# Performance work log

Measured on AMD Instinct MI355X. Metric: run time of the kernel, lower is better.

## Reference

```python
import jax, jax.numpy as jnp
import numpy as np

N_ENS = 4        # number of FGL sub-layers
B, N_IN, N_OUT = 1, 16384, 4096
IN_C, OUT_C = 16, 16
DENSITY = 0.10   # sparsity proxy for A + dA random perturbation


def setup_inputs() -> dict:
    key = jax.random.key(0)
    kx, ka, km, kw, kb = jax.random.split(key, 5)
    x = jax.random.normal(kx, (B, N_IN, IN_C), dtype=jnp.float32)
    # Dense storage of the n perturbed sparse adjacencies A_i (n_out, n_in)
    A_vals = jax.random.normal(ka, (N_ENS, N_OUT, N_IN), dtype=jnp.float32)
    A_mask = jax.random.bernoulli(km, DENSITY, (N_ENS, N_OUT, N_IN))
    As = A_vals * A_mask.astype(jnp.float32)
    Ws = jax.random.normal(kw, (N_ENS, IN_C, OUT_C), dtype=jnp.float32) * (1.0 / np.sqrt(IN_C))
    bs = jax.random.normal(kb, (N_ENS, OUT_C), dtype=jnp.float32) * 0.01
    return {"x": x, "As": As, "Ws": Ws, "bs": bs}


def reference(x, As, Ws, bs):
    # Each FGL_i: y_i = (A_i @ x) @ W_i + b_i
    # x: [b, n_in, f]; As: [n, n_out, n_in]; Ws: [n, f, g]; bs: [n, g]
    h = jnp.einsum('noi,bif->nbof', As, x)            # graph aggregation per ensemble member
    y = jnp.einsum('nbof,nfg->nbog', h, Ws)           # per-member linear transform
    y = y + bs[:, None, None, :]
    return jnp.mean(y, axis=0)                        # sum over n members / n
```

## Files before the change

### kernel.cpp

```cpp
#include <hip/hip_runtime.h>


#define N_ENS 4
#define N_OUT 4096
#define N_IN  16384
#define ROWS  (N_ENS * N_OUT)
#define GSPLIT 32
#define ICHUNK (N_IN / GSPLIT)

__global__ __launch_bounds__(256, 6) void k_main(const float* __restrict__ A,
                                                 const float* __restrict__ x,
                                                 float* __restrict__ hp) {
    const int split  = blockIdx.x & (GSPLIT - 1);
    const int rowblk = blockIdx.x >> 5;
    const int row = rowblk * 256 + threadIdx.x;
    const int i0 = split * ICHUNK;

    const float* Ap  = A + (size_t)row * N_IN + i0;
    const float* xp0 = x + (size_t)i0 * 16;

    float acc[16];
#pragma unroll
    for (int f = 0; f < 16; ++f) acc[f] = 0.0f;

    for (int s = 0; s < ICHUNK / 16; ++s) {
        float4 av4[4];
#pragma unroll
        for (int q = 0; q < 4; ++q)
            av4[q] = *(const float4*)(Ap + s * 16 + q * 4);
        const float* af = (const float*)av4;
        const float* xp = xp0 + (size_t)s * 256;

#pragma unroll
        for (int ii = 0; ii < 16; ++ii) {
            const float av = af[ii];
#pragma unroll
            for (int f = 0; f < 16; ++f)
                acc[f] = fmaf(av, xp[ii * 16 + f], acc[f]);
        }
    }

    float* outp = hp + ((size_t)split * ROWS + row) * 16;
#pragma unroll
    for (int f = 0; f < 16; ++f) outp[f] = acc[f];
}

__global__ __launch_bounds__(256) void k_hsum(const float* __restrict__ hp,
                                              float* __restrict__ h) {
    int t = blockIdx.x * 256 + threadIdx.x;
    float s = 0.0f;
#pragma unroll
    for (int sp = 0; sp < GSPLIT; ++sp)
        s += hp[(size_t)sp * (ROWS * 16) + t];
    h[t] = s;
}

__global__ __launch_bounds__(256) void k_out(const float* __restrict__ h,
                                             const float* __restrict__ Ws,
                                             const float* __restrict__ bs,
                                             float* __restrict__ out) {
    __shared__ float Wsm[N_ENS * 16 * 16];
    __shared__ float bsm[N_ENS * 16];
    int tid = threadIdx.x;
#pragma unroll
    for (int r = 0; r < 4; ++r) Wsm[tid + 256 * r] = Ws[tid + 256 * r];
    if (tid < 64) bsm[tid] = bs[tid];
    __syncthreads();

    int idx = blockIdx.x * 256 + tid;
    int o = idx >> 4;
    int gg = idx & 15;
    float s = 0.0f;
#pragma unroll
    for (int n = 0; n < N_ENS; ++n) {
        const float* hr = h + ((size_t)(n * N_OUT + o) << 4);
        float t = 0.0f;
#pragma unroll
        for (int f = 0; f < 16; ++f)
            t = fmaf(hr[f], Wsm[n * 256 + f * 16 + gg], t);
        s += t + bsm[n * 16 + gg];
    }
    out[idx] = 0.25f * s;
}

extern "C" void kernel_launch(void* const* d_in, const int* in_sizes, int n_in,
                              void* d_out, int out_size, void* d_ws, size_t ws_size,
                              hipStream_t stream) {
    const float* x  = (const float*)d_in[0];
    const float* As = (const float*)d_in[1];
    const float* Ws = (const float*)d_in[2];
    const float* bs = (const float*)d_in[3];
    float* out = (float*)d_out;

    float* hp = (float*)d_ws;
    float* h  = (float*)((char*)d_ws + (size_t)32 * 1024 * 1024);

    k_main<<<64 * GSPLIT, 256, 0, stream>>>(As, x, hp);
    k_hsum<<<(ROWS * 16) / 256, 256, 0, stream>>>(hp, h);
    k_out<<<(N_OUT * 16) / 256, 256, 0, stream>>>(h, Ws, bs, out);
}
```

Baseline: 1.415 ms.

## Split each row across four lanes and reduce split count for partial sums

Remaps k_main so four lanes cooperate on one adjacency row, each loading a float4 slice, then combines the partial accumulators with wave shuffles. It reduces the i-dimension split from 32 to 8, which shrinks the partial-sum buffer written by k_main and read by k_hsum. x is read as float4 vectors. The cost is extra shuffle work and a per-lane branch to select the output slice.

```diff
diff --git a/kernel.cpp b/kernel.cpp
--- a/kernel.cpp
+++ b/kernel.cpp
@@ -5,44 +5,59 @@
 #define N_OUT 4096
 #define N_IN  16384
 #define ROWS  (N_ENS * N_OUT)
-#define GSPLIT 32
+#define GSPLIT 8
 #define ICHUNK (N_IN / GSPLIT)
+#define NSTEP  (ICHUNK / 16)
 
-__global__ __launch_bounds__(256, 6) void k_main(const float* __restrict__ A,
+__global__ __launch_bounds__(256, 4) void k_main(const float* __restrict__ A,
                                                  const float* __restrict__ x,
                                                  float* __restrict__ hp) {
-    const int split  = blockIdx.x & (GSPLIT - 1);
-    const int rowblk = blockIdx.x >> 5;
-    const int row = rowblk * 256 + threadIdx.x;
-    const int i0 = split * ICHUNK;
+    const int split   = blockIdx.x & (GSPLIT - 1);
+    const int rowtile = blockIdx.x >> 3;
+    const int tid  = threadIdx.x;
+    const int wave = tid >> 6;
+    const int r    = (tid >> 2) & 15;
+    const int p    = tid & 3;
 
-    const float* Ap  = A + (size_t)row * N_IN + i0;
-    const float* xp0 = x + (size_t)i0 * 16;
+    const int row = rowtile * 64 + wave * 16 + r;
+    const int i0  = split * ICHUNK;
+
+    const float* Ap = A + (size_t)row * N_IN + i0 + (p << 2);
 
     float acc[16];
 #pragma unroll
     for (int f = 0; f < 16; ++f) acc[f] = 0.0f;
 
-    for (int s = 0; s < ICHUNK / 16; ++s) {
-        float4 av4[4];
+    for (int s = 0; s < NSTEP; ++s) {
+        float4 av = *(const float4*)(Ap + s * 16);
+        const float* xb = x + ((size_t)(i0 + s * 16 + (p << 2)) << 4);
+        const float* af = (const float*)&av;
 #pragma unroll
-        for (int q = 0; q < 4; ++q)
-            av4[q] = *(const float4*)(Ap + s * 16 + q * 4);
-        const float* af = (const float*)av4;
-        const float* xp = xp0 + (size_t)s * 256;
-
+        for (int q = 0; q < 4; ++q) {
+            const float a = af[q];
 #pragma unroll
-        for (int ii = 0; ii < 16; ++ii) {
-            const float av = af[ii];
-#pragma unroll
-            for (int f = 0; f < 16; ++f)
-                acc[f] = fmaf(av, xp[ii * 16 + f], acc[f]);
+            for (int j = 0; j < 4; ++j) {
+                float4 xv = *(const float4*)(xb + (q << 4) + (j << 2));
+                acc[4 * j + 0] = fmaf(a, xv.x, acc[4 * j + 0]);
+                acc[4 * j + 1] = fmaf(a, xv.y, acc[4 * j + 1]);
+                acc[4 * j + 2] = fmaf(a, xv.z, acc[4 * j + 2]);
+                acc[4 * j + 3] = fmaf(a, xv.w, acc[4 * j + 3]);
+            }
         }
     }
 
-    float* outp = hp + ((size_t)split * ROWS + row) * 16;
 #pragma unroll
-    for (int f = 0; f < 16; ++f) outp[f] = acc[f];
+    for (int f = 0; f < 16; ++f) {
+        acc[f] += __shfl_xor(acc[f], 1, 64);
+        acc[f] += __shfl_xor(acc[f], 2, 64);
+    }
+
+    float4 v;
+    if      (p == 0) v = make_float4(acc[0],  acc[1],  acc[2],  acc[3]);
+    else if (p == 1) v = make_float4(acc[4],  acc[5],  acc[6],  acc[7]);
+    else if (p == 2) v = make_float4(acc[8],  acc[9],  acc[10], acc[11]);
+    else             v = make_float4(acc[12], acc[13], acc[14], acc[15]);
+    *(float4*)(hp + (((size_t)split * ROWS + row) << 4) + (p << 2)) = v;
 }
 
 __global__ __launch_bounds__(256) void k_hsum(const float* __restrict__ hp,
@@ -93,9 +108,9 @@
     float* out = (float*)d_out;
 
     float* hp = (float*)d_ws;
-    float* h  = (float*)((char*)d_ws + (size_t)32 * 1024 * 1024);
+    float* h  = (float*)((char*)d_ws + (size_t)8 * 1024 * 1024);
 
-    k_main<<<64 * GSPLIT, 256, 0, stream>>>(As, x, hp);
+    k_main<<<256 * GSPLIT, 256, 0, stream>>>(As, x, hp);
     k_hsum<<<(ROWS * 16) / 256, 256, 0, stream>>>(hp, h);
     k_out<<<(N_OUT * 16) / 256, 256, 0, stream>>>(h, Ws, bs, out);
 }
```

Measured after the change: 2.894 ms. 104% more time.

## Stage x chunk in LDS and remap threads to 4 rows by 4 features

Applied to the files above, without the earlier changes.

The main GEMV-like kernel now copies its 512x16 slice of x into shared memory once per block. Each lane computes 4 rows by 4 output features instead of one row by 16, reading A with float4 loads and prefetching the next step into registers. This is meant to cut redundant global reads of x and spread the accumulators across lanes. The trade is a 32KB LDS footprint and a lower occupancy hint (4 instead of 6). Each wave's A reads are now strided across 16 rows, which may hurt coalescing.

```diff
diff --git a/kernel.cpp b/kernel.cpp
--- a/kernel.cpp
+++ b/kernel.cpp
@@ -7,42 +7,79 @@
 #define ROWS  (N_ENS * N_OUT)
 #define GSPLIT 32
 #define ICHUNK (N_IN / GSPLIT)
+#define NSTEP  (ICHUNK / 4)
 
-__global__ __launch_bounds__(256, 6) void k_main(const float* __restrict__ A,
+__global__ __launch_bounds__(256, 4) void k_main(const float* __restrict__ A,
                                                  const float* __restrict__ x,
                                                  float* __restrict__ hp) {
-    const int split  = blockIdx.x & (GSPLIT - 1);
-    const int rowblk = blockIdx.x >> 5;
-    const int row = rowblk * 256 + threadIdx.x;
-    const int i0 = split * ICHUNK;
+    __shared__ float xs[ICHUNK * 16];
 
-    const float* Ap  = A + (size_t)row * N_IN + i0;
-    const float* xp0 = x + (size_t)i0 * 16;
+    const int split   = blockIdx.x & (GSPLIT - 1);
+    const int rowblk  = blockIdx.x >> 5;
+    const int tid  = threadIdx.x;
+    const int i0   = split * ICHUNK;
 
-    float acc[16];
+    {
+        const float4* xg = (const float4*)(x + (size_t)i0 * 16);
+        float4* xs4 = (float4*)xs;
 #pragma unroll
-    for (int f = 0; f < 16; ++f) acc[f] = 0.0f;
+        for (int j = 0; j < 8; ++j)
+            xs4[tid + 256 * j] = xg[tid + 256 * j];
+    }
+    __syncthreads();
 
-    for (int s = 0; s < ICHUNK / 16; ++s) {
-        float4 av4[4];
+    const int wave  = tid >> 6;
+    const int lane  = tid & 63;
+    const int o_sub = lane & 15;
+    const int f_sub = lane >> 4;
+    const int rowbase = rowblk * 256 + wave * 64 + o_sub;
+
+    const float* Ap = A + (size_t)rowbase * N_IN + i0;
+
+    float4 acc[4];
+#pragma unroll
+    for (int k = 0; k < 4; ++k) acc[k] = make_float4(0.f, 0.f, 0.f, 0.f);
+
+    float4 a_cur[4], a_nxt[4];
+#pragma unroll
+    for (int k = 0; k < 4; ++k)
+        a_cur[k] = *(const float4*)(Ap + (size_t)k * 16 * N_IN);
+
+#pragma unroll 2
+    for (int s = 0; s < NSTEP; ++s) {
+        if (s + 1 < NSTEP) {
+#pragma unroll
+            for (int k = 0; k < 4; ++k)
+                a_nxt[k] = *(const float4*)(Ap + (size_t)k * 16 * N_IN + (s + 1) * 4);
+        }
+
+        float4 xv[4];
 #pragma unroll
         for (int q = 0; q < 4; ++q)
-            av4[q] = *(const float4*)(Ap + s * 16 + q * 4);
-        const float* af = (const float*)av4;
-        const float* xp = xp0 + (size_t)s * 256;
+            xv[q] = *(const float4*)&xs[(s * 4 + q) * 16 + f_sub * 4];
 
 #pragma unroll
-        for (int ii = 0; ii < 16; ++ii) {
-            const float av = af[ii];
+        for (int k = 0; k < 4; ++k) {
+            const float* af = (const float*)&a_cur[k];
 #pragma unroll
-            for (int f = 0; f < 16; ++f)
-                acc[f] = fmaf(av, xp[ii * 16 + f], acc[f]);
+            for (int q = 0; q < 4; ++q) {
+                const float a = af[q];
+                acc[k].x = fmaf(a, xv[q].x, acc[k].x);
+                acc[k].y = fmaf(a, xv[q].y, acc[k].y);
+                acc[k].z = fmaf(a, xv[q].z, acc[k].z);
+                acc[k].w = fmaf(a, xv[q].w, acc[k].w);
+            }
         }
+
+#pragma unroll
+        for (int k = 0; k < 4; ++k) a_cur[k] = a_nxt[k];
     }
 
-    float* outp = hp + ((size_t)split * ROWS + row) * 16;
 #pragma unroll
-    for (int f = 0; f < 16; ++f) outp[f] = acc[f];
+    for (int k = 0; k < 4; ++k) {
+        int row = rowbase + 16 * k;
+        *(float4*)(hp + (((size_t)split * ROWS + row) << 4) + (f_sub << 2)) = acc[k];
+    }
 }
 
 __global__ __launch_bounds__(256) void k_hsum(const float* __restrict__ hp,
```

New measurement: 1.682 ms. 18.8% more time.
